# Kernel tuning notes

Measured on AMD Instinct MI355X. Metric: run time of the kernel, lower is better.

## Reference

```python
import jax, jax.numpy as jnp
import numpy as np

N_BITS = 4
SIZE_SCALE = 8 // N_BITS  # 2 int4 values per byte
MASK = (1 << N_BITS) - 1  # 0xF

OC, IC = 8192, 8192
B = 64


def setup_inputs() -> dict:
    key = jax.random.key(0)
    k_in, k_w, k_d, k_z, k_b = jax.random.split(key, 5)
    input = jax.random.normal(k_in, (B, IC), dtype=jnp.float32)
    # packed uint8 weight buffer: [OC // SIZE_SCALE, IC]; stored as int32 with byte values
    weight_packed = jax.random.randint(k_w, (OC // SIZE_SCALE, IC), 0, 256, dtype=jnp.int32)
    # per-output-channel affine quant params
    delta = jax.random.uniform(k_d, (OC,), dtype=jnp.float32) * 0.01 + 1e-4
    zero_point = jax.random.uniform(k_z, (OC,), dtype=jnp.float32) * MASK
    bias = jax.random.normal(k_b, (OC,), dtype=jnp.float32)
    return {"input": input, "weight_packed": weight_packed, "delta": delta,
            "zero_point": zero_point, "bias": bias}


def _dequantize(weight_packed, delta, zero_point):
    # Bit-unpack: each byte holds SIZE_SCALE values of N_BITS each, packed along
    # the output-channel dim (dim 0), low nibble first.
    parts = [ (weight_packed >> (N_BITS * i)) & MASK for i in range(SIZE_SCALE) ]
    w_int = jnp.concatenate(parts, axis=0)               # [OC, IC] int
    # Affine dequant, per output channel: w = (q - zp) * delta
    w = (w_int.astype(jnp.float32) - zero_point[:, None]) * delta[:, None]
    return w


def reference(input, weight_packed, delta, zero_point, bias):
    # use_weight_quant=True, use_act_quant=False (defaults in the module)
    w = _dequantize(weight_packed, delta, zero_point)    # [OC, IC]
    out = jnp.dot(input, w.T) + bias                     # F.linear
    return out
```

## Files before the change

### kernel.cpp

```cpp
#include <hip/hip_runtime.h>

constexpr int BATCH = 64;
constexpr int IC    = 8192;
constexpr int OC    = 8192;
constexpr int OCH   = 4096;
constexpr int KSPLIT = 4;
constexpr int KPER  = IC / KSPLIT;
constexpr int BK    = 128;
constexpr int NITER = KPER / BK;
constexpr int LDK   = BK + 8;

typedef __bf16 bf16x8 __attribute__((ext_vector_type(8)));
typedef float  f32x4  __attribute__((ext_vector_type(4)));
typedef int    i32x4  __attribute__((ext_vector_type(4)));

static __device__ __forceinline__ unsigned short f2bf(float f) {
    unsigned u = __float_as_uint(f);
    u += 0x7FFFu + ((u >> 16) & 1u);
    return (unsigned short)(u >> 16);
}

static __device__ __forceinline__ unsigned pack2bf(int n0, int n1) {
    unsigned f0 = __float_as_uint((float)n0);
    unsigned f1 = __float_as_uint((float)n1);
    return __builtin_amdgcn_perm(f1, f0, 0x07060302u);
}

__global__ __launch_bounds__(256) void prep_kernel(
    const float* __restrict__ in, unsigned short* __restrict__ Abf,
    float* __restrict__ S4)
{
    const int b   = blockIdx.x;
    const int row = b >> 2;
    const int q   = b & 3;
    const int t   = threadIdx.x;
    const float*          rp = in  + (size_t)row * IC + q * 2048;
    unsigned short*       op = Abf + (size_t)row * IC + q * 2048;

    float sum = 0.f;
#pragma unroll
    for (int i = 0; i < 2; ++i) {
        const int c = i * 1024 + t * 4;
        const float4 v = *(const float4*)(rp + c);
        sum += (v.x + v.y) + (v.z + v.w);
        ushort4 o = make_ushort4(f2bf(v.x), f2bf(v.y), f2bf(v.z), f2bf(v.w));
        *(ushort4*)(op + c) = o;
    }
#pragma unroll
    for (int off = 32; off > 0; off >>= 1) sum += __shfl_down(sum, off);

    __shared__ float red[4];
    if ((t & 63) == 0) red[t >> 6] = sum;
    __syncthreads();
    if (t == 0) S4[row * 4 + q] = (red[0] + red[1]) + (red[2] + red[3]);
}

__global__ __launch_bounds__(512, 4) void gemm_kernel(
    const unsigned short* __restrict__ Abf,
    const int* __restrict__ wp,
    float* __restrict__ part)
{
    __shared__ unsigned short lA[2][64 * LDK];
    __shared__ unsigned short lW[2][64 * LDK];

    const int t    = threadIdx.x;
    const int lane = t & 63;
    const int lm   = lane & 15;
    const int lq   = lane >> 4;
    const int wv   = (t >> 6) & 3;
    const int kh   = t >> 8;

    const int nt  = blockIdx.x & 127;
    const int ks  = blockIdx.x >> 7;
    const int r0  = nt * 32;
    const int kb0 = ks * KPER;

    f32x4 acc[4];
    const f32x4 zero4 = {0.f, 0.f, 0.f, 0.f};
#pragma unroll
    for (int i = 0; i < 4; ++i) acc[i] = zero4;

    const int uAr = t >> 3, uAc = (t & 7) * 16;
    const int uWr = t >> 4, uWc = (t & 15) * 8;

    const unsigned short* pA = Abf + (size_t)uAr * IC + kb0 + uAc;
    const int*            pW = wp  + (size_t)(r0 + uWr) * IC + kb0 + uWc;

    const int sAo   = uAr * LDK + uAc;
    const int sWoLo = uWr * LDK + uWc;
    const int sWoHi = (uWr + 32) * LDK + uWc;
    const int fBo   = (wv * 16 + lm) * LDK + kh * 64 + lq * 8;
    const int fAo   = lm * LDK + kh * 64 + lq * 8;

    i32x4 aA0, aA1, wA0, wA1;
    i32x4 aB0, aB1, wB0, wB1;

#define KBAR() { asm volatile("s_waitcnt lgkmcnt(0)" ::: "memory"); \
                 __builtin_amdgcn_s_barrier(); }

#define LOADG(sa0, sa1, sw0, sw1, koff)                                  \
    sa0 = *(const i32x4*)(pA + (koff));                                  \
    sa1 = *(const i32x4*)(pA + (koff) + 8);                              \
    sw0 = __builtin_nontemporal_load((const i32x4*)(pW + (koff)));       \
    sw1 = __builtin_nontemporal_load((const i32x4*)(pW + (koff) + 4));

#define STAGE(buf, sa0, sa1, sw0, sw1) {             \
    *(i32x4*)(&lA[buf][sAo])     = sa0;              \
    *(i32x4*)(&lA[buf][sAo + 8]) = sa1;              \
    i32x4 lo_, hi_;                                  \
    lo_[0] = pack2bf(sw0[0] & 15, sw0[1] & 15);      \
    lo_[1] = pack2bf(sw0[2] & 15, sw0[3] & 15);      \
    lo_[2] = pack2bf(sw1[0] & 15, sw1[1] & 15);      \
    lo_[3] = pack2bf(sw1[2] & 15, sw1[3] & 15);      \
    hi_[0] = pack2bf(sw0[0] >> 4, sw0[1] >> 4);      \
    hi_[1] = pack2bf(sw0[2] >> 4, sw0[3] >> 4);      \
    hi_[2] = pack2bf(sw1[0] >> 4, sw1[1] >> 4);      \
    hi_[3] = pack2bf(sw1[2] >> 4, sw1[3] >> 4);      \
    *(i32x4*)(&lW[buf][sWoLo]) = lo_;                \
    *(i32x4*)(&lW[buf][sWoHi]) = hi_; }

#define MM(p) {                                                                   \
    _Pragma("unroll")                                                             \
    for (int s = 0; s < 2; ++s) {                                                 \
        const bf16x8 bfrg = *(const bf16x8*)(&lW[p][fBo + s * 32]);               \
        _Pragma("unroll")                                                         \
        for (int mt = 0; mt < 4; ++mt) {                                          \
            const bf16x8 afrg = *(const bf16x8*)(&lA[p][fAo + mt * 16 * LDK + s * 32]); \
            acc[mt] = __builtin_amdgcn_mfma_f32_16x16x32_bf16(afrg, bfrg, acc[mt], 0, 0, 0); \
        } } }

    LOADG(aA0, aA1, wA0, wA1, 0);
    LOADG(aB0, aB1, wB0, wB1, BK);
    STAGE(0, aA0, aA1, wA0, wA1);
    KBAR();

    for (int it2 = 0; it2 < (NITER - 2) / 2; ++it2) {
        {
            const int koff = (2 * it2 + 2) * BK;
            LOADG(aA0, aA1, wA0, wA1, koff);
            MM(0);
            STAGE(1, aB0, aB1, wB0, wB1);
            KBAR();
        }
        {
            const int koff = (2 * it2 + 3) * BK;
            LOADG(aB0, aB1, wB0, wB1, koff);
            MM(1);
            STAGE(0, aA0, aA1, wA0, wA1);
            KBAR();
        }
    }
    MM(0);
    STAGE(1, aB0, aB1, wB0, wB1);
    KBAR();
    MM(1);

#undef LOADG
#undef STAGE
#undef MM
#undef KBAR

    __syncthreads();
    f32x4* lR = (f32x4*)(&lA[0][0]);
    const int o = (wv * 64 + lane) << 2;
    if (kh) {
#pragma unroll
        for (int mt = 0; mt < 4; ++mt) lR[o + mt] = acc[mt];
    }
    __syncthreads();
    if (!kh) {
#pragma unroll
        for (int mt = 0; mt < 4; ++mt) acc[mt] += lR[o + mt];

        const int cr = wv * 16 + lm;
        const int ch = (cr < 32) ? (r0 + cr) : (OCH + r0 + (cr - 32));
        float* pout = part + (size_t)ks * (BATCH * OC) + ch;

#pragma unroll
        for (int mt = 0; mt < 4; ++mt) {
#pragma unroll
            for (int r = 0; r < 4; ++r) {
                const int m = mt * 16 + lq * 4 + r;
                pout[(size_t)m * OC] = acc[mt][r];
            }
        }
    }
}

__global__ __launch_bounds__(256) void reduce_kernel(
    const float* __restrict__ part,
    const float* __restrict__ delta,
    const float* __restrict__ zp,
    const float* __restrict__ bias,
    const float* __restrict__ S4,
    float* __restrict__ out)
{
    const int e  = (blockIdx.x * 256 + threadIdx.x) * 4;
    const int m  = e >> 13;
    const int ch = e & (OC - 1);

    float4 s = {0.f, 0.f, 0.f, 0.f};
#pragma unroll
    for (int k = 0; k < KSPLIT; ++k) {
        const float4 p = *(const float4*)(part + (size_t)k * (BATCH * OC) + e);
        s.x += p.x; s.y += p.y; s.z += p.z; s.w += p.w;
    }
    const float4 d = *(const float4*)(delta + ch);
    const float4 z = *(const float4*)(zp + ch);
    const float4 b = *(const float4*)(bias + ch);
    const float Sm = (S4[m * 4 + 0] + S4[m * 4 + 1]) + (S4[m * 4 + 2] + S4[m * 4 + 3]);

    float4 o;
    o.x = d.x * s.x + b.x - d.x * z.x * Sm;
    o.y = d.y * s.y + b.y - d.y * z.y * Sm;
    o.z = d.z * s.z + b.z - d.z * z.z * Sm;
    o.w = d.w * s.w + b.w - d.w * z.w * Sm;
    *(float4*)(out + e) = o;
}

extern "C" void kernel_launch(void* const* d_in, const int* in_sizes, int n_in,
                              void* d_out, int out_size, void* d_ws, size_t ws_size,
                              hipStream_t stream) {
    const float* input = (const float*)d_in[0];
    const int*   wpk   = (const int*)d_in[1];
    const float* delta = (const float*)d_in[2];
    const float* zp    = (const float*)d_in[3];
    const float* bias  = (const float*)d_in[4];
    float* out = (float*)d_out;

    unsigned short* Abf = (unsigned short*)d_ws;
    float* S4   = (float*)((char*)d_ws + (size_t)BATCH * IC * 2);
    float* part = (float*)((char*)d_ws + (size_t)BATCH * IC * 2 + 4096);

    prep_kernel<<<dim3(256), dim3(256), 0, stream>>>(input, Abf, S4);
    gemm_kernel<<<dim3(128 * KSPLIT), dim3(512), 0, stream>>>(Abf, wpk, part);
    reduce_kernel<<<dim3(BATCH * OC / 1024), dim3(256), 0, stream>>>(part, delta, zp, bias, S4, out);
}
```

Before: 208.5 us.

## Replace split-K partial buffer and reduce kernel with atomic accumulation into output

Removes the partial-sum workspace and the separate reduce kernel. A new init kernel writes the bias and zero-point correction into the output first, and the GEMM kernel then atomically adds delta-scaled partial sums from each K split. The MFMA tiling per wave also changes from a 1x4 layout to a 2x2 layout, which reduces LDS fragment loads per MFMA. The cost is float atomics (four-way contention per output element) and a nondeterministic summation order.

```diff
diff --git a/kernel.cpp b/kernel.cpp
--- a/kernel.cpp
+++ b/kernel.cpp
@@ -55,10 +55,35 @@
     if (t == 0) S4[row * 4 + q] = (red[0] + red[1]) + (red[2] + red[3]);
 }
 
+__global__ __launch_bounds__(256) void init_kernel(
+    const float* __restrict__ delta,
+    const float* __restrict__ zp,
+    const float* __restrict__ bias,
+    const float* __restrict__ S4,
+    float* __restrict__ out)
+{
+    const int e  = (blockIdx.x * 256 + threadIdx.x) * 4;
+    const int m  = e >> 13;
+    const int ch = e & (OC - 1);
+
+    const float4 d = *(const float4*)(delta + ch);
+    const float4 z = *(const float4*)(zp + ch);
+    const float4 b = *(const float4*)(bias + ch);
+    const float Sm = (S4[m * 4 + 0] + S4[m * 4 + 1]) + (S4[m * 4 + 2] + S4[m * 4 + 3]);
+
+    float4 o;
+    o.x = b.x - d.x * z.x * Sm;
+    o.y = b.y - d.y * z.y * Sm;
+    o.z = b.z - d.z * z.z * Sm;
+    o.w = b.w - d.w * z.w * Sm;
+    *(float4*)(out + e) = o;
+}
+
 __global__ __launch_bounds__(512, 4) void gemm_kernel(
     const unsigned short* __restrict__ Abf,
     const int* __restrict__ wp,
-    float* __restrict__ part)
+    const float* __restrict__ delta,
+    float* __restrict__ out)
 {
     __shared__ unsigned short lA[2][64 * LDK];
     __shared__ unsigned short lW[2][64 * LDK];
@@ -67,18 +92,22 @@
     const int lane = t & 63;
     const int lm   = lane & 15;
     const int lq   = lane >> 4;
-    const int wv   = (t >> 6) & 3;
-    const int kh   = t >> 8;
+    const int wv   = t >> 6;
+    const int kh   = wv >> 2;
+    const int mq   = (wv >> 1) & 1;
+    const int nq   = wv & 1;
 
     const int nt  = blockIdx.x & 127;
     const int ks  = blockIdx.x >> 7;
     const int r0  = nt * 32;
     const int kb0 = ks * KPER;
 
-    f32x4 acc[4];
+    f32x4 acc[2][2];
     const f32x4 zero4 = {0.f, 0.f, 0.f, 0.f};
 #pragma unroll
-    for (int i = 0; i < 4; ++i) acc[i] = zero4;
+    for (int i = 0; i < 2; ++i)
+#pragma unroll
+        for (int j = 0; j < 2; ++j) acc[i][j] = zero4;
 
     const int uAr = t >> 3, uAc = (t & 7) * 16;
     const int uWr = t >> 4, uWc = (t & 15) * 8;
@@ -89,8 +118,8 @@
     const int sAo   = uAr * LDK + uAc;
     const int sWoLo = uWr * LDK + uWc;
     const int sWoHi = (uWr + 32) * LDK + uWc;
-    const int fBo   = (wv * 16 + lm) * LDK + kh * 64 + lq * 8;
-    const int fAo   = lm * LDK + kh * 64 + lq * 8;
+    const int fAo   = (mq * 32 + lm) * LDK + kh * 64 + lq * 8;
+    const int fBo   = (nq * 32 + lm) * LDK + kh * 64 + lq * 8;
 
     i32x4 aA0, aA1, wA0, wA1;
     i32x4 aB0, aB1, wB0, wB1;
@@ -122,12 +151,15 @@
 #define MM(p) {                                                                   \
     _Pragma("unroll")                                                             \
     for (int s = 0; s < 2; ++s) {                                                 \
-        const bf16x8 bfrg = *(const bf16x8*)(&lW[p][fBo + s * 32]);               \
-        _Pragma("unroll")                                                         \
-        for (int mt = 0; mt < 4; ++mt) {                                          \
-            const bf16x8 afrg = *(const bf16x8*)(&lA[p][fAo + mt * 16 * LDK + s * 32]); \
-            acc[mt] = __builtin_amdgcn_mfma_f32_16x16x32_bf16(afrg, bfrg, acc[mt], 0, 0, 0); \
-        } } }
+        const bf16x8 b0 = *(const bf16x8*)(&lW[p][fBo + s * 32]);                 \
+        const bf16x8 b1 = *(const bf16x8*)(&lW[p][fBo + 16 * LDK + s * 32]);      \
+        const bf16x8 a0 = *(const bf16x8*)(&lA[p][fAo + s * 32]);                 \
+        const bf16x8 a1 = *(const bf16x8*)(&lA[p][fAo + 16 * LDK + s * 32]);      \
+        acc[0][0] = __builtin_amdgcn_mfma_f32_16x16x32_bf16(a0, b0, acc[0][0], 0, 0, 0); \
+        acc[0][1] = __builtin_amdgcn_mfma_f32_16x16x32_bf16(a0, b1, acc[0][1], 0, 0, 0); \
+        acc[1][0] = __builtin_amdgcn_mfma_f32_16x16x32_bf16(a1, b0, acc[1][0], 0, 0, 0); \
+        acc[1][1] = __builtin_amdgcn_mfma_f32_16x16x32_bf16(a1, b1, acc[1][1], 0, 0, 0); \
+    } }
 
     LOADG(aA0, aA1, wA0, wA1, 0);
     LOADG(aB0, aB1, wB0, wB1, BK);
@@ -162,60 +194,35 @@
 
     __syncthreads();
     f32x4* lR = (f32x4*)(&lA[0][0]);
-    const int o = (wv * 64 + lane) << 2;
+    const int o = ((wv & 3) * 64 + lane) << 2;
     if (kh) {
-#pragma unroll
-        for (int mt = 0; mt < 4; ++mt) lR[o + mt] = acc[mt];
+        lR[o + 0] = acc[0][0];
+        lR[o + 1] = acc[0][1];
+        lR[o + 2] = acc[1][0];
+        lR[o + 3] = acc[1][1];
     }
     __syncthreads();
     if (!kh) {
-#pragma unroll
-        for (int mt = 0; mt < 4; ++mt) acc[mt] += lR[o + mt];
-
-        const int cr = wv * 16 + lm;
-        const int ch = (cr < 32) ? (r0 + cr) : (OCH + r0 + (cr - 32));
-        float* pout = part + (size_t)ks * (BATCH * OC) + ch;
-
-#pragma unroll
-        for (int mt = 0; mt < 4; ++mt) {
-#pragma unroll
-            for (int r = 0; r < 4; ++r) {
-                const int m = mt * 16 + lq * 4 + r;
-                pout[(size_t)m * OC] = acc[mt][r];
+        acc[0][0] += lR[o + 0];
+        acc[0][1] += lR[o + 1];
+        acc[1][0] += lR[o + 2];
+        acc[1][1] += lR[o + 3];
+
+#pragma unroll
+        for (int nt2 = 0; nt2 < 2; ++nt2) {
+            const int ch = (nq ? OCH : 0) + r0 + nt2 * 16 + lm;
+            const float d = delta[ch];
+            float* po = out + ch;
+#pragma unroll
+            for (int mt2 = 0; mt2 < 2; ++mt2) {
+#pragma unroll
+                for (int r = 0; r < 4; ++r) {
+                    const int m = mq * 32 + mt2 * 16 + lq * 4 + r;
+                    atomicAdd(po + (size_t)m * OC, d * acc[mt2][nt2][r]);
+                }
             }
         }
     }
-}
-
-__global__ __launch_bounds__(256) void reduce_kernel(
-    const float* __restrict__ part,
-    const float* __restrict__ delta,
-    const float* __restrict__ zp,
-    const float* __restrict__ bias,
-    const float* __restrict__ S4,
-    float* __restrict__ out)
-{
-    const int e  = (blockIdx.x * 256 + threadIdx.x) * 4;
-    const int m  = e >> 13;
-    const int ch = e & (OC - 1);
-
-    float4 s = {0.f, 0.f, 0.f, 0.f};
-#pragma unroll
-    for (int k = 0; k < KSPLIT; ++k) {
-        const float4 p = *(const float4*)(part + (size_t)k * (BATCH * OC) + e);
-        s.x += p.x; s.y += p.y; s.z += p.z; s.w += p.w;
-    }
-    const float4 d = *(const float4*)(delta + ch);
-    const float4 z = *(const float4*)(zp + ch);
-    const float4 b = *(const float4*)(bias + ch);
-    const float Sm = (S4[m * 4 + 0] + S4[m * 4 + 1]) + (S4[m * 4 + 2] + S4[m * 4 + 3]);
-
-    float4 o;
-    o.x = d.x * s.x + b.x - d.x * z.x * Sm;
-    o.y = d.y * s.y + b.y - d.y * z.y * Sm;
-    o.z = d.z * s.z + b.z - d.z * z.z * Sm;
-    o.w = d.w * s.w + b.w - d.w * z.w * Sm;
-    *(float4*)(out + e) = o;
 }
 
 extern "C" void kernel_launch(void* const* d_in, const int* in_sizes, int n_in,
@@ -230,9 +237,8 @@
 
     unsigned short* Abf = (unsigned short*)d_ws;
     float* S4   = (float*)((char*)d_ws + (size_t)BATCH * IC * 2);
-    float* part = (float*)((char*)d_ws + (size_t)BATCH * IC * 2 + 4096);
 
     prep_kernel<<<dim3(256), dim3(256), 0, stream>>>(input, Abf, S4);
-    gemm_kernel<<<dim3(128 * KSPLIT), dim3(512), 0, stream>>>(Abf, wpk, part);
-    reduce_kernel<<<dim3(BATCH * OC / 1024), dim3(256), 0, stream>>>(part, delta, zp, bias, S4, out);
-}
+    init_kernel<<<dim3(BATCH * OC / 1024), dim3(256), 0, stream>>>(delta, zp, bias, S4, out);
+    gemm_kernel<<<dim3(128 * KSPLIT), dim3(512), 0, stream>>>(Abf, wpk, delta, out);
+}
```

Measured after the change: 208.6 us. No clear change (+0.0%).
